# Optimization experiments

Measured on AMD Instinct MI355X. Metric: run time of the kernel, lower is better.

The kernel has to match this reference:

```python
import jax, jax.numpy as jnp
import numpy as np

NEG_SLOPE = 0.2
LN_EPS = 1e-5


def setup_inputs() -> dict:
    key = jax.random.key(0)
    k1, k2, k3, k4 = jax.random.split(key, 4)
    B, K, D, H = 64, 256, 1024, 2
    x = jax.random.normal(k1, (B, K, D), dtype=jnp.float32)
    adj = jax.random.randint(k2, (K, K), 0, 2, dtype=jnp.int32)
    # Xavier-ish scaling for weights
    W = jax.random.normal(k3, (D, D), dtype=jnp.float32) * (1.0 / np.sqrt(D))
    a = jax.random.normal(k4, (H, 2 * D), dtype=jnp.float32) * (1.0 / np.sqrt(2 * D))
    gamma = jnp.ones((D,), dtype=jnp.float32)
    beta = jnp.zeros((D,), dtype=jnp.float32)
    return {"x": x, "adj": adj, "W": W, "a": a, "gamma": gamma, "beta": beta}


def _layer_norm(y, gamma, beta):
    mu = jnp.mean(y, axis=-1, keepdims=True)
    var = jnp.mean(jnp.square(y - mu), axis=-1, keepdims=True)
    return (y - mu) * jax.lax.rsqrt(var + LN_EPS) * gamma + beta


def reference(x, adj, W, a, gamma, beta):
    # x: (B,K,D), adj: (K,K), W: (D,D), a: (H,2D)
    D = W.shape[1]
    h = jnp.einsum("bki,io->bko", x, W)  # (B,K,D)
    # GAT trick: a^T [h_i; h_j] = a_src . h_i + a_dst . h_j (same math as
    # the huge pairwise-concat + Linear in the original module).
    a_src, a_dst = a[:, :D], a[:, D:]  # each (H,D)
    f_i = jnp.einsum("bkd,hd->bhk", h, a_src)  # (B,H,K)
    f_j = jnp.einsum("bkd,hd->bhk", h, a_dst)  # (B,H,K)
    e = f_i[:, :, :, None] + f_j[:, :, None, :]  # (B,H,K,K)
    e = jnp.where(e >= 0, e, NEG_SLOPE * e)  # LeakyReLU
    mask = (adj != 0)[None, None]  # (1,1,K,K)
    e = jnp.where(mask, e, -jnp.inf)
    attn = jax.nn.softmax(e, axis=-1)
    attn = jnp.where(jnp.isnan(attn), 0.0, attn)  # nan_to_num for all-masked rows
    # dropout is identity in eval mode
    head_out = jnp.einsum("bhij,bjd->bhid", attn, h)  # (B,H,K,D)
    out = jnp.mean(head_out, axis=1)  # average heads, (B,K,D)
    out = _layer_norm(out + x, gamma, beta)  # residual is Identity (in_dim==out_dim)
    return out
```

## Files before the change

### kernel.cpp

```cpp
#include <hip/hip_runtime.h>
#include <hip/hip_bf16.h>

#define KN 256
#define DD 1024
#define HH 2

typedef __attribute__((ext_vector_type(8))) short short8;
typedef __attribute__((ext_vector_type(4))) float f32x4;

__device__ __forceinline__ ushort f2b(float f) {
  union { float f; unsigned u; } v; v.f = f;
  unsigned u = v.u;
  return (ushort)((u + 0x7fffu + ((u >> 16) & 1u)) >> 16);
}
__device__ __forceinline__ float b2f(ushort h) {
  union { unsigned u; float f; } v; v.u = ((unsigned)h) << 16;
  return v.f;
}
__device__ __forceinline__ void gload16(const ushort* g, ushort* l) {
  __builtin_amdgcn_global_load_lds(
      (const __attribute__((address_space(1))) void*)g,
      (__attribute__((address_space(3))) void*)l, 16, 0, 0);
}

__global__ __launch_bounds__(256) void k_prep(const float* __restrict__ x,
                                              ushort* __restrict__ xb,
                                              const float* __restrict__ W,
                                              ushort* __restrict__ WTb) {
  int bid = blockIdx.x, tid = threadIdx.x;
  if (bid < 2048) {
    int c0 = bid * 256 + tid;
    for (int it = 0; it < 4; ++it) {
      size_t i = ((size_t)c0 + (size_t)it * 524288) * 8;
      float4 v0 = *reinterpret_cast<const float4*>(&x[i]);
      float4 v1 = *reinterpret_cast<const float4*>(&x[i + 4]);
      short8 o;
      o[0] = (short)f2b(v0.x); o[1] = (short)f2b(v0.y);
      o[2] = (short)f2b(v0.z); o[3] = (short)f2b(v0.w);
      o[4] = (short)f2b(v1.x); o[5] = (short)f2b(v1.y);
      o[6] = (short)f2b(v1.z); o[7] = (short)f2b(v1.w);
      *reinterpret_cast<short8*>(&xb[i]) = o;
    }
  } else {
    __shared__ float t[32][33];
    int wb = bid - 2048;
    int bx = wb & 31, by = wb >> 5;
    int tx = tid & 31, ty = tid >> 5;
    int xx = bx * 32 + tx;
    int y0 = by * 32 + ty;
    for (int i = 0; i < 32; i += 8)
      t[ty + i][tx] = W[(size_t)(y0 + i) * DD + xx];
    __syncthreads();
    int xo = by * 32 + tx;
    int yo = bx * 32 + ty;
    for (int i = 0; i < 32; i += 8)
      WTb[(size_t)(yo + i) * DD + xo] = f2b(t[tx][ty + i]);
  }
}

__global__ __launch_bounds__(512, 2) void k_gemm_h(const ushort* __restrict__ xb,
                                                   const ushort* __restrict__ WTb,
                                                   ushort* __restrict__ hT) {
  __shared__ ushort As[2][16384];
  __shared__ ushort Bs[2][16384];
  const int tid = threadIdx.x;
  const int w = tid >> 6, lane = tid & 63;
  const int flat = blockIdx.x;
  const int bn = (flat >> 3) & 3;
  const int b  = (flat & 7) + 8 * (flat >> 5);
  const int wm = (w >> 2) * 128, wn = (w & 3) * 64;
  const int r16 = lane & 15, kqi = lane >> 4;
  const ushort* gA0 = xb + (size_t)(b * 256) * DD;
  const ushort* gB0 = WTb + (size_t)(bn * 256) * DD;
  const int srow0 = tid >> 3;
  const int scc   = (tid & 7) ^ ((tid >> 3) & 7);
  const int sdst0 = (tid & ~63) * 8;
  const int cs0 = (kqi)     ^ (r16 & 7);
  const int cs1 = (kqi + 4) ^ (r16 & 7);
  f32x4 acc[8][4] = {};
  short8 bfv[4][2];

#define STG(ISB, BUF, H, KB)                                                    \
  {                                                                             \
    const ushort* g0_ = (ISB) ? gB0 : gA0;                                      \
    ushort* l0_ = (ISB) ? Bs[BUF] : As[BUF];                                    \
    gload16(g0_ + (size_t)((H) * 128 + srow0) * DD + (KB) + scc * 8,            \
            l0_ + (H) * 8192 + sdst0);                                          \
    gload16(g0_ + (size_t)((H) * 128 + 64 + srow0) * DD + (KB) + scc * 8,       \
            l0_ + (H) * 8192 + 4096 + sdst0);                                   \
  }

#define PHASE(Q, BUF, LOADB, WMODE, STAGE_STMT)                                 \
  {                                                                             \
    short8 af0[2], af1[2];                                                      \
    {                                                                           \
      const ushort* Ab_ = As[BUF];                                              \
      int ra_ = (wm + (Q) * 32 + r16) * 64;                                     \
      int rb_ = (wm + (Q) * 32 + 16 + r16) * 64;                                \
      af0[0] = *(const short8*)(Ab_ + ra_ + cs0 * 8);                           \
      af0[1] = *(const short8*)(Ab_ + ra_ + cs1 * 8);                           \
      af1[0] = *(const short8*)(Ab_ + rb_ + cs0 * 8);                           \
      af1[1] = *(const short8*)(Ab_ + rb_ + cs1 * 8);                           \
    }                                                                           \
    if (LOADB) {                                                                \
      const ushort* Bb_ = Bs[BUF];                                              \
      _Pragma("unroll")                                                         \
      for (int nf = 0; nf < 4; ++nf) {                                          \
        int rn_ = (wn + nf * 16 + r16) * 64;                                    \
        bfv[nf][0] = *(const short8*)(Bb_ + rn_ + cs0 * 8);                     \
        bfv[nf][1] = *(const short8*)(Bb_ + rn_ + cs1 * 8);                     \
      }                                                                         \
    }                                                                           \
    STAGE_STMT;                                                                 \
    __builtin_amdgcn_s_barrier();                                               \
    asm volatile("s_waitcnt lgkmcnt(0)" ::: "memory");                          \
    __builtin_amdgcn_sched_barrier(0);                                          \
    __builtin_amdgcn_s_setprio(1);                                              \
    _Pragma("unroll")                                                           \
    for (int nf = 0; nf < 4; ++nf) {                                            \
      acc[(Q)*2][nf]   = __builtin_amdgcn_mfma_f32_16x16x32_bf16(af0[0], bfv[nf][0], acc[(Q)*2][nf], 0, 0, 0);     \
      acc[(Q)*2+1][nf] = __builtin_amdgcn_mfma_f32_16x16x32_bf16(af1[0], bfv[nf][0], acc[(Q)*2+1][nf], 0, 0, 0);   \
    }                                                                           \
    _Pragma("unroll")                                                           \
    for (int nf = 0; nf < 4; ++nf) {                                            \
      acc[(Q)*2][nf]   = __builtin_amdgcn_mfma_f32_16x16x32_bf16(af0[1], bfv[nf][1], acc[(Q)*2][nf], 0, 0, 0);     \
      acc[(Q)*2+1][nf] = __builtin_amdgcn_mfma_f32_16x16x32_bf16(af1[1], bfv[nf][1], acc[(Q)*2+1][nf], 0, 0, 0);   \
    }                                                                           \
    __builtin_amdgcn_s_setprio(0);                                              \
    __builtin_amdgcn_sched_barrier(0);                                          \
    if ((WMODE) == 1) { asm volatile("s_waitcnt vmcnt(6)" ::: "memory"); }      \
    else if ((WMODE) == 2) { asm volatile("s_waitcnt vmcnt(0)" ::: "memory"); } \
    __builtin_amdgcn_s_barrier();                                               \
  }

  STG(1, 0, 0, 0) STG(1, 0, 1, 0) STG(0, 0, 0, 0) STG(0, 0, 1, 0)
  STG(1, 1, 0, 64) STG(1, 1, 1, 64) STG(0, 1, 0, 64)
  asm volatile("s_waitcnt vmcnt(6)" ::: "memory");
  __builtin_amdgcn_sched_barrier(0);
  __builtin_amdgcn_s_barrier();

  for (int i = 0; i < 8; ++i) {
    const int k1 = i * 128 + 64;
    const int k2 = i * 128 + 128;
    const int k3 = i * 128 + 192;
    const bool s2 = (k2 < 1024), s3 = (k3 < 1024);
    const int wt = (i < 7) ? 1 : 2;
    PHASE(0, 0, 1, 0,  { STG(0, 1, 1, k1) })
    PHASE(1, 0, 0, 0,  { if (s2) STG(1, 0, 0, k2) })
    PHASE(2, 0, 0, 0,  { if (s2) STG(1, 0, 1, k2) })
    PHASE(3, 0, 0, wt, { if (s2) STG(0, 0, 0, k2) })
    PHASE(0, 1, 1, 0,  { if (s2) STG(0, 0, 1, k2) })
    PHASE(1, 1, 0, 0,  { if (s3) STG(1, 1, 0, k3) })
    PHASE(2, 1, 0, 0,  { if (s3) STG(1, 1, 1, k3) })
    PHASE(3, 1, 0, wt, { if (s3) STG(0, 1, 0, k3) })
  }
#undef PHASE
#undef STG

  const int g = lane >> 4;
  #pragma unroll
  for (int mf = 0; mf < 8; ++mf) {
    int j0 = wm + mf * 16 + g * 4;
    #pragma unroll
    for (int nf = 0; nf < 4; ++nf) {
      int C = bn * 256 + wn + nf * 16 + r16;
      ushort4 o;
      o.x = f2b(acc[mf][nf][0]); o.y = f2b(acc[mf][nf][1]);
      o.z = f2b(acc[mf][nf][2]); o.w = f2b(acc[mf][nf][3]);
      *reinterpret_cast<ushort4*>(&hT[((size_t)b * DD + C) * KN + j0]) = o;
    }
  }
}

__global__ __launch_bounds__(256) void k_f(const ushort* __restrict__ hT,
                                           const float* __restrict__ a,
                                           float* __restrict__ fip, float* __restrict__ fjp) {
  __shared__ float als[4][256];
  int b = blockIdx.x, dq = blockIdx.y;
  int tid = threadIdx.x;
  for (int v = 0; v < 4; ++v) als[v][tid] = a[v * DD + dq * 256 + tid];
  __syncthreads();
  const ushort* base = hT + ((size_t)b * DD + dq * 256) * KN + tid;
  float a0 = 0.f, a1 = 0.f, a2 = 0.f, a3 = 0.f;
  #pragma unroll 8
  for (int d = 0; d < 256; ++d) {
    float hv = b2f(base[(size_t)d * KN]);
    a0 += hv * als[0][d];
    a1 += hv * als[1][d];
    a2 += hv * als[2][d];
    a3 += hv * als[3][d];
  }
  size_t o = ((size_t)(dq * 64 + b) * HH) * KN + tid;
  fip[o] = a0;
  fjp[o] = a1;
  fip[o + KN] = a2;
  fjp[o + KN] = a3;
}

__global__ __launch_bounds__(256) void k_attn(const float* __restrict__ fip, const float* __restrict__ fjp,
                                              const int* __restrict__ adj, ushort* __restrict__ Pb) {
  int w = threadIdx.x >> 6, l = threadIdx.x & 63;
  int gw = blockIdx.x * 4 + w;
  int b = gw >> 8, i = gw & 255;
  int4 am = *reinterpret_cast<const int4*>(adj + i * KN + l * 4);
  int msk[4] = { am.x, am.y, am.z, am.w };
  float fi0 = 0.f, fi1 = 0.f;
  float fj0[4] = {0.f, 0.f, 0.f, 0.f}, fj1[4] = {0.f, 0.f, 0.f, 0.f};
  for (int dq = 0; dq < 4; ++dq) {
    size_t o = ((size_t)(dq * 64 + b) * HH) * KN;
    fi0 += fip[o + i];
    fi1 += fip[o + KN + i];
    float4 t0 = *reinterpret_cast<const float4*>(&fjp[o + l * 4]);
    float4 t1 = *reinterpret_cast<const float4*>(&fjp[o + KN + l * 4]);
    fj0[0] += t0.x; fj0[1] += t0.y; fj0[2] += t0.z; fj0[3] += t0.w;
    fj1[0] += t1.x; fj1[1] += t1.y; fj1[2] += t1.z; fj1[3] += t1.w;
  }
  float e0[4], e1[4];
  const float NEGINF = -3.0e38f;
  float m0 = NEGINF, m1 = NEGINF;
  for (int e = 0; e < 4; ++e) {
    float v0 = fi0 + fj0[e], v1 = fi1 + fj1[e];
    v0 = v0 >= 0.f ? v0 : 0.2f * v0;
    v1 = v1 >= 0.f ? v1 : 0.2f * v1;
    e0[e] = v0; e1[e] = v1;
    if (msk[e]) { m0 = fmaxf(m0, v0); m1 = fmaxf(m1, v1); }
  }
  for (int off = 1; off < 64; off <<= 1) {
    m0 = fmaxf(m0, __shfl_xor(m0, off));
    m1 = fmaxf(m1, __shfl_xor(m1, off));
  }
  float p0[4], p1[4], s0 = 0.f, s1 = 0.f;
  for (int e = 0; e < 4; ++e) {
    p0[e] = msk[e] ? __expf(e0[e] - m0) : 0.f;
    p1[e] = msk[e] ? __expf(e1[e] - m1) : 0.f;
    s0 += p0[e]; s1 += p1[e];
  }
  for (int off = 1; off < 64; off <<= 1) {
    s0 += __shfl_xor(s0, off);
    s1 += __shfl_xor(s1, off);
  }
  float i0 = s0 > 0.f ? 1.f / s0 : 0.f;
  float i1 = s1 > 0.f ? 1.f / s1 : 0.f;
  ushort4 o;
  o.x = f2b(0.5f * (p0[0] * i0 + p1[0] * i1));
  o.y = f2b(0.5f * (p0[1] * i0 + p1[1] * i1));
  o.z = f2b(0.5f * (p0[2] * i0 + p1[2] * i1));
  o.w = f2b(0.5f * (p0[3] * i0 + p1[3] * i1));
  *reinterpret_cast<ushort4*>(&Pb[((size_t)b * KN + i) * KN + l * 4]) = o;
}

__global__ __launch_bounds__(512) void k_gemm_o_ln(const ushort* __restrict__ Pb,
                                                   const ushort* __restrict__ hT,
                                                   const ushort* __restrict__ xb,
                                                   const float* __restrict__ gamma,
                                                   const float* __restrict__ beta,
                                                   float* __restrict__ out) {
  __shared__ ushort As[1024];
  __shared__ ushort Bs[32768];
  __shared__ float red[32][8][2];
  const int tid = threadIdx.x;
  const int w = tid >> 6, lane = tid & 63;
  const int flat = blockIdx.x;
  const int itile = (flat >> 3) & 7;
  const int b = (flat & 7) + 8 * (flat >> 6);
  const int wn = w * 128;
  const int r16 = lane & 15, kqi = lane >> 4, g = lane >> 4;
  const ushort* PbB = Pb + ((size_t)b * KN + itile * 32) * KN;
  const ushort* hTB = hT + (size_t)b * DD * KN;
  f32x4 acc[2][8] = {};
  const int wb = tid & ~63;

  #define OSTAGE(kt)                                                               \
    {                                                                              \
      _Pragma("unroll")                                                            \
      for (int s = 0; s < 8; ++s) {                                                \
        int c = s * 512 + tid;                                                     \
        int row = c >> 2, kc = c & 3;                                              \
        int kcs = kc ^ ((row >> 1) & 3);                                           \
        gload16(hTB + (size_t)row * KN + (kt) + kcs * 8,                           \
                Bs + (size_t)(s * 512 + wb) * 8);                                  \
      }                                                                            \
      {                                                                            \
        int c = w * 16 + lane;                                                     \
        int row = c >> 2, kc = c & 3;                                              \
        int kcs = kc ^ ((row >> 1) & 3);                                           \
        if (lane < 16)                                                             \
          gload16(PbB + (size_t)row * KN + (kt) + kcs * 8, As + w * 128);          \
      }                                                                            \
    }

  for (int it = 0; it < 8; ++it) {
    OSTAGE(it * 32);
    asm volatile("s_waitcnt vmcnt(0)" ::: "memory");
    __builtin_amdgcn_s_barrier();
    __builtin_amdgcn_sched_barrier(0);
    short8 af[2];
    #pragma unroll
    for (int mf = 0; mf < 2; ++mf) {
      int row = mf * 16 + r16;
      af[mf] = *reinterpret_cast<const short8*>(As + row * 32 + (kqi ^ ((row >> 1) & 3)) * 8);
    }
    #pragma unroll
    for (int nf = 0; nf < 8; ++nf) {
      int row = wn + nf * 16 + r16;
      short8 bf = *reinterpret_cast<const short8*>(Bs + (size_t)row * 32 + (kqi ^ ((row >> 1) & 3)) * 8);
      acc[0][nf] = __builtin_amdgcn_mfma_f32_16x16x32_bf16(af[0], bf, acc[0][nf], 0, 0, 0);
      acc[1][nf] = __builtin_amdgcn_mfma_f32_16x16x32_bf16(af[1], bf, acc[1][nf], 0, 0, 0);
    }
    __builtin_amdgcn_sched_barrier(0);
    __builtin_amdgcn_s_barrier();
  }
  #undef OSTAGE

  float ps[2][4] = {}, qs[2][4] = {};
  #pragma unroll
  for (int mf = 0; mf < 2; ++mf)
    #pragma unroll
    for (int nf = 0; nf < 8; ++nf) {
      int col = wn + nf * 16 + r16;
      #pragma unroll
      for (int rr = 0; rr < 4; ++rr) {
        int row = mf * 16 + g * 4 + rr;
        size_t gi = ((size_t)(b * KN + itile * 32 + row)) * DD + col;
        float v = acc[mf][nf][rr] + b2f(xb[gi]);
        acc[mf][nf][rr] = v;
        ps[mf][rr] += v; qs[mf][rr] += v * v;
      }
    }
  #pragma unroll
  for (int off = 1; off < 16; off <<= 1)
    #pragma unroll
    for (int mf = 0; mf < 2; ++mf)
      #pragma unroll
      for (int rr = 0; rr < 4; ++rr) {
        ps[mf][rr] += __shfl_xor(ps[mf][rr], off);
        qs[mf][rr] += __shfl_xor(qs[mf][rr], off);
      }
  if (r16 == 0) {
    #pragma unroll
    for (int mf = 0; mf < 2; ++mf)
      #pragma unroll
      for (int rr = 0; rr < 4; ++rr) {
        int row = mf * 16 + g * 4 + rr;
        red[row][w][0] = ps[mf][rr];
        red[row][w][1] = qs[mf][rr];
      }
  }
  __syncthreads();
  float mu_[2][4], inv_[2][4];
  #pragma unroll
  for (int mf = 0; mf < 2; ++mf)
    #pragma unroll
    for (int rr = 0; rr < 4; ++rr) {
      int row = mf * 16 + g * 4 + rr;
      float S = 0.f, Q = 0.f;
      #pragma unroll
      for (int wv = 0; wv < 8; ++wv) { S += red[row][wv][0]; Q += red[row][wv][1]; }
      float m = S * (1.0f / DD);
      float var = Q * (1.0f / DD) - m * m;
      mu_[mf][rr] = m;
      inv_[mf][rr] = rsqrtf(var + 1e-5f);
    }
  #pragma unroll
  for (int nf = 0; nf < 8; ++nf) {
    int col = wn + nf * 16 + r16;
    float gm = gamma[col], bt = beta[col];
    #pragma unroll
    for (int mf = 0; mf < 2; ++mf)
      #pragma unroll
      for (int rr = 0; rr < 4; ++rr) {
        int row = mf * 16 + g * 4 + rr;
        size_t gi = ((size_t)(b * KN + itile * 32 + row)) * DD + col;
        out[gi] = (acc[mf][nf][rr] - mu_[mf][rr]) * inv_[mf][rr] * gm + bt;
      }
  }
}

extern "C" void kernel_launch(void* const* d_in, const int* in_sizes, int n_in,
                              void* d_out, int out_size, void* d_ws, size_t ws_size,
                              hipStream_t stream) {
  const float* x     = (const float*)d_in[0];
  const int*   adj   = (const int*)d_in[1];
  const float* W     = (const float*)d_in[2];
  const float* a     = (const float*)d_in[3];
  const float* gamma = (const float*)d_in[4];
  const float* beta  = (const float*)d_in[5];
  float* out = (float*)d_out;

  char* ws = (char*)d_ws;
  const size_t OFS_WT = 0;
  const size_t OFS_XB = 2097152;
  const size_t OFS_HT = 35651584;
  const size_t OFS_PB = 69206016;
  const size_t NEED   = 77856768;
  if (ws_size < NEED) return;

  ushort* WTb   = (ushort*)(ws + OFS_WT);
  float*  fip   = (float*)(ws + OFS_WT);
  float*  fjp   = (float*)(ws + OFS_WT + 524288);
  ushort* xb    = (ushort*)(ws + OFS_XB);
  ushort* hT    = (ushort*)(ws + OFS_HT);
  ushort* Pb    = (ushort*)(ws + OFS_PB);

  k_prep<<<3072, 256, 0, stream>>>(x, xb, W, WTb);
  k_gemm_h<<<256, 512, 0, stream>>>(xb, WTb, hT);
  k_f<<<dim3(64, 4), 256, 0, stream>>>(hT, a, fip, fjp);
  k_attn<<<4096, 256, 0, stream>>>(fip, fjp, adj, Pb);
  k_gemm_o_ln<<<512, 512, 0, stream>>>(Pb, hT, xb, gamma, beta, out);
}
```

Baseline: 123.9 us.

## Stage full P tile in LDS once and read hT fragments directly from global

The output GEMM kernel no longer stages hT tiles through a 64KB shared buffer with a barrier every k-step. Instead the whole 32x256 P tile is loaded into LDS once with a swizzle, and B fragments are read from global memory straight into registers. This removes the per-iteration barriers and most of the LDS traffic, and lowers LDS use enough that more blocks may fit per CU. In exchange, global reads of hT are strided and uncoalesced (16B per lane across rows) and rely on cache hits, with no latency hiding from explicit staging.

```diff
diff --git a/kernel.cpp b/kernel.cpp
--- a/kernel.cpp
+++ b/kernel.cpp
@@ -255,8 +255,7 @@
                                                    const float* __restrict__ gamma,
                                                    const float* __restrict__ beta,
                                                    float* __restrict__ out) {
-  __shared__ ushort As[1024];
-  __shared__ ushort Bs[32768];
+  __shared__ ushort As[8192];
   __shared__ float red[32][8][2];
   const int tid = threadIdx.x;
   const int w = tid >> 6, lane = tid & 63;
@@ -270,47 +269,33 @@
   f32x4 acc[2][8] = {};
   const int wb = tid & ~63;
 
-  #define OSTAGE(kt)                                                               \
-    {                                                                              \
-      _Pragma("unroll")                                                            \
-      for (int s = 0; s < 8; ++s) {                                                \
-        int c = s * 512 + tid;                                                     \
-        int row = c >> 2, kc = c & 3;                                              \
-        int kcs = kc ^ ((row >> 1) & 3);                                           \
-        gload16(hTB + (size_t)row * KN + (kt) + kcs * 8,                           \
-                Bs + (size_t)(s * 512 + wb) * 8);                                  \
-      }                                                                            \
-      {                                                                            \
-        int c = w * 16 + lane;                                                     \
-        int row = c >> 2, kc = c & 3;                                              \
-        int kcs = kc ^ ((row >> 1) & 3);                                           \
-        if (lane < 16)                                                             \
-          gload16(PbB + (size_t)row * KN + (kt) + kcs * 8, As + w * 128);          \
-      }                                                                            \
-    }
+  #pragma unroll
+  for (int s = 0; s < 2; ++s) {
+    int c = s * 512 + tid;
+    int row = c >> 5, kc = c & 31;
+    int kcs = kc ^ (row & 7);
+    gload16(PbB + (size_t)row * KN + kcs * 8, As + (size_t)(s * 512 + wb) * 8);
+  }
+  asm volatile("s_waitcnt vmcnt(0)" ::: "memory");
+  __builtin_amdgcn_s_barrier();
 
   for (int it = 0; it < 8; ++it) {
-    OSTAGE(it * 32);
-    asm volatile("s_waitcnt vmcnt(0)" ::: "memory");
-    __builtin_amdgcn_s_barrier();
-    __builtin_amdgcn_sched_barrier(0);
+    const int kt = it * 32;
     short8 af[2];
     #pragma unroll
     for (int mf = 0; mf < 2; ++mf) {
       int row = mf * 16 + r16;
-      af[mf] = *reinterpret_cast<const short8*>(As + row * 32 + (kqi ^ ((row >> 1) & 3)) * 8);
+      int chunk = ((it * 4 + kqi) ^ (row & 7));
+      af[mf] = *reinterpret_cast<const short8*>(As + row * 256 + chunk * 8);
     }
     #pragma unroll
     for (int nf = 0; nf < 8; ++nf) {
       int row = wn + nf * 16 + r16;
-      short8 bf = *reinterpret_cast<const short8*>(Bs + (size_t)row * 32 + (kqi ^ ((row >> 1) & 3)) * 8);
+      short8 bf = *reinterpret_cast<const short8*>(hTB + (size_t)row * KN + kt + kqi * 8);
       acc[0][nf] = __builtin_amdgcn_mfma_f32_16x16x32_bf16(af[0], bf, acc[0][nf], 0, 0, 0);
       acc[1][nf] = __builtin_amdgcn_mfma_f32_16x16x32_bf16(af[1], bf, acc[1][nf], 0, 0, 0);
     }
-    __builtin_amdgcn_sched_barrier(0);
-    __builtin_amdgcn_s_barrier();
-  }
-  #undef OSTAGE
+  }
 
   float ps[2][4] = {}, qs[2][4] = {};
   #pragma unroll
```

After: 128.6 us. 1.04x slower.
